# Optimization experiments

Hardware: AMD Instinct MI355X
Metric: run time of the kernel (lower is better)

Reference implementation:

```python
import jax, jax.numpy as jnp
import numpy as np

# Loihi CUBA neuron constants (from netParams['neuron']):
# threshold theta = vThMant * 2^6, decays out of 4096, weighted input scaled by 2^6.
THETA = 80.0 * 64.0
I_DECAY = 1024.0
V_DECAY = 128.0
W_SCALE = 64.0
SURR_BETA = THETA  # width of surrogate-gradient window (SLAYER-style exp pdf)

@jax.custom_jvp
def spike_fn(v):
    return (v >= THETA).astype(v.dtype)

@spike_fn.defjvp
def spike_fn_jvp(primals, tangents):
    (v,), (dv,) = primals, tangents
    s = (v >= THETA).astype(v.dtype)
    grad = jnp.exp(-jnp.abs(v - THETA) / SURR_BETA) / SURR_BETA
    return s, grad * dv

def loihi_neuron(wx):
    """Leaky integrate-and-fire (Loihi CUBA) dynamics over time.
    wx: (B, C, T) weighted input; returns (B, C, T) spikes."""
    a_i = (4096.0 - I_DECAY) / 4096.0
    a_v = (4096.0 - V_DECAY) / 4096.0
    xT = jnp.moveaxis(wx, -1, 0)  # (T, B, C)
    def step(carry, x_t):
        cur, vol = carry
        cur = a_i * cur + W_SCALE * x_t
        vol = a_v * vol + cur
        s = spike_fn(vol)
        vol = vol * (1.0 - s)  # reset on spike (refDelay = 1)
        return (cur, vol), s
    z = jnp.zeros(xT.shape[1:], wx.dtype)
    _, sT = jax.lax.scan(step, (z, z), xT)
    return jnp.moveaxis(sT, 0, -1)

def delay_shift(s, d=1):
    # shift spikes by d time steps (axonal delay), zero-padded at t=0
    zeros = jnp.zeros(s.shape[:-1] + (d,), s.dtype)
    return jnp.concatenate([zeros, s[..., :-d]], axis=-1)

def setup_inputs() -> dict:
    key = jax.random.key(0)
    k1, k2, k3 = jax.random.split(key, 3)
    B, Nin, Nhid, Nout, T = 64, 512, 1024, 512, 1024
    x = (jax.random.uniform(k1, (B, Nin, T)) < 0.1).astype(jnp.float32)
    w1 = jax.random.normal(k2, (Nhid, Nin), jnp.float32) * 0.3
    w2 = jax.random.normal(k3, (Nout, Nhid), jnp.float32) * 0.3
    return {"x": x, "w1": w1, "w2": w2}

def reference(x, w1, w2):
    h = jnp.einsum('bit,hi->bht', x, w1)           # fc1 per time step
    s1 = delay_shift(loihi_neuron(h), 1)            # spikeLoihi + delayShift(1)
    o = jnp.einsum('bht,oh->bot', s1, w2)           # fc2 per time step
    return delay_shift(loihi_neuron(o), 1)
```

## Files before the change

kernel.cpp:

```cpp
#include <hip/hip_runtime.h>
#include <stdint.h>

#define NB   64
#define NIN  512
#define NHID 1024
#define NOUT 512
#define NT   1024

#define LSTRIDE 128

#define A_I   0.75f
#define A_V   0.96875f
#define WSC   64.0f
#define THETA 5120.0f

typedef uint32_t u32x4 __attribute__((ext_vector_type(4)));
typedef uint32_t u32x2 __attribute__((ext_vector_type(2)));

#define GL4(DST, PTR, OFF) \
  asm volatile("global_load_dwordx4 %0, %1, off offset:" OFF : "=v"(DST) : "v"(PTR))
#define GL2(DST, PTR) \
  asm volatile("global_load_dwordx2 %0, %1, off" : "=v"(DST) : "v"(PTR))
#define GL1(DST, PTR) \
  asm volatile("global_load_dword %0, %1, off" : "=v"(DST) : "v"(PTR))

#define LDS_FENCE() asm volatile("s_waitcnt lgkmcnt(0)" ::: "memory")

__global__ void __launch_bounds__(256) k_bits1(const float* __restrict__ x,
                                               uint32_t* __restrict__ bits1) {
  int blk = blockIdx.x;
  int b  = blk >> 6;
  int iw = (blk >> 2) & 15;
  int tc = blk & 3;
  int t  = tc * 256 + threadIdx.x;
  const float* xp = x + ((size_t)(b * NIN + iw * 32)) * NT + t;
  uint32_t w = 0;
#pragma unroll
  for (int j = 0; j < 32; ++j) {
    float v = xp[(size_t)j * NT];
    if (v > 0.5f) w |= (1u << j);
  }
  bits1[((size_t)b * NT + t) * 16 + iw] = w;
}

__global__ void __launch_bounds__(256) k_extract(const uint64_t* __restrict__ bits,
                                                 uint32_t* __restrict__ cnt,
                                                 uint16_t* __restrict__ list,
                                                 int words, int sentinel_scaled,
                                                 int shift) {
  int gid = blockIdx.x * 256 + threadIdx.x;
  const uint64_t* wp = bits + (size_t)gid * words;
  uint16_t* lp = list + (size_t)gid * LSTRIDE;
  int c = 0;
  for (int w = 0; w < words; ++w) {
    uint64_t v = wp[w];
    while (v) {
      int j = __builtin_ctzll(v);
      v &= v - 1;
      if (c < LSTRIDE) lp[c] = (uint16_t)(((w << 6) + j) << shift);
      ++c;
    }
  }
  if (c > LSTRIDE) c = LSTRIDE;
  cnt[gid] = (uint32_t)((c + 15) >> 4);
  int cp = c;
  if (cp & 1) { lp[cp] = (uint16_t)sentinel_scaled; ++cp; }
  uint32_t s2 = (uint32_t)sentinel_scaled * 0x10001u;
  uint32_t* lp32 = (uint32_t*)lp;
  for (int k = cp >> 1; k < LSTRIDE / 2; ++k) lp32[k] = s2;
}

#define SUM16(ACC, B) do { _Pragma("unroll") \
  for (int q_ = 0; q_ < 16; ++q_) (ACC) += (B)[q_]; } while (0)
#define SUM8(ACC, B) do { _Pragma("unroll") \
  for (int q_ = 0; q_ < 8; ++q_) (ACC) += (B)[q_]; } while (0)

__global__ void __launch_bounds__(1024, 4) k_fc1(const float* __restrict__ w1,
                                                 const uint32_t* __restrict__ cnt1,
                                                 const uint16_t* __restrict__ list1,
                                                 uint64_t* __restrict__ bits2) {
  extern __shared__ float lds[];
  int xcd = blockIdx.x & 7, slot = blockIdx.x >> 3;
  int bq = (xcd << 1) | (slot & 1);
  int hq = slot >> 1;
  int h0 = hq * 64;
  for (int idx = threadIdx.x; idx < NIN * 64; idx += 1024) {
    int hl = idx >> 9;
    int i  = idx & (NIN - 1);
    lds[i * 64 + hl] = w1[(size_t)(h0 + hl) * NIN + i];
  }
  if (threadIdx.x < 64) lds[NIN * 64 + threadIdx.x] = 0.0f;
  float* stbase = lds + 32832;
  int*   flbase = (int*)(lds + 32832 + 2048);
  stbase[threadIdx.x]        = 0.0f;
  stbase[1024 + threadIdx.x] = 0.0f;
  if (threadIdx.x < 16)
    flbase[threadIdx.x] = (int)(threadIdx.x >> 2) - 4;
  __syncthreads();

  int wid = threadIdx.x >> 6, lane = threadIdx.x & 63;
  int c   = wid & 3;
  int par = wid >> 2;
  int b = bq * 4 + c;
  size_t bt = (size_t)b * NT;
  float2* stMine = (float2*)(stbase + (par * 4 + c) * 128);
  float2* stPart = (float2*)(stbase + (((par + 3) & 3) * 4 + c) * 128);
  volatile int* flMine = flbase + par * 4 + c;
  volatile int* flPart = flbase + ((par + 3) & 3) * 4 + c;

  float P[16], Q[16], R[16];
  u32x4 ct[8], rt[8];
  int cntC;
  {
    const u32x4* Lp = (const u32x4*)(list1 + (bt + par) * LSTRIDE);
#pragma unroll
    for (int k = 0; k < 8; ++k) ct[k] = Lp[k];
    cntC = (int)cnt1[bt + par];
  }

#define FC1_LOADG(BUF, CA_, CB_) do {                                           \
    u32x4 ca_ = (CA_), cb_ = (CB_);                                             \
    BUF[0]  = lds[(ca_[0] & 0xffffu) + lane];                                   \
    BUF[1]  = lds[(ca_[0] >> 16)     + lane];                                   \
    BUF[2]  = lds[(ca_[1] & 0xffffu) + lane];                                   \
    BUF[3]  = lds[(ca_[1] >> 16)     + lane];                                   \
    BUF[4]  = lds[(ca_[2] & 0xffffu) + lane];                                   \
    BUF[5]  = lds[(ca_[2] >> 16)     + lane];                                   \
    BUF[6]  = lds[(ca_[3] & 0xffffu) + lane];                                   \
    BUF[7]  = lds[(ca_[3] >> 16)     + lane];                                   \
    BUF[8]  = lds[(cb_[0] & 0xffffu) + lane];                                   \
    BUF[9]  = lds[(cb_[0] >> 16)     + lane];                                   \
    BUF[10] = lds[(cb_[1] & 0xffffu) + lane];                                   \
    BUF[11] = lds[(cb_[1] >> 16)     + lane];                                   \
    BUF[12] = lds[(cb_[2] & 0xffffu) + lane];                                   \
    BUF[13] = lds[(cb_[2] >> 16)     + lane];                                   \
    BUF[14] = lds[(cb_[3] & 0xffffu) + lane];                                   \
    BUF[15] = lds[(cb_[3] >> 16)     + lane];                                   \
  } while (0)

#define FC1_JOIN(RT, CW)                                                        \
    asm volatile("s_waitcnt vmcnt(0)"                                           \
      : "+v"(RT[0]), "+v"(RT[1]), "+v"(RT[2]), "+v"(RT[3]),                     \
        "+v"(RT[4]), "+v"(RT[5]), "+v"(RT[6]), "+v"(RT[7]), "+v"(CW)            \
      :: "memory")

#define FC1_BODY(T, CT, RT) do {                                                \
    const int t_ = (T);                                                         \
    int tp_ = t_ + 4;  if (tp_ > NT - 1) tp_ = NT - 1;                          \
    const uint16_t* lp_ = list1 + (bt + tp_) * LSTRIDE;                         \
    const uint32_t* cp_ = cnt1 + (bt + tp_);                                    \
    uint32_t cw_;                                                               \
    GL1(cw_, cp_);                                                              \
    GL4(RT[0], lp_, "0");   GL4(RT[1], lp_, "16");                              \
    GL4(RT[2], lp_, "32");  GL4(RT[3], lp_, "48");                              \
    GL4(RT[4], lp_, "64");  GL4(RT[5], lp_, "80");                              \
    GL4(RT[6], lp_, "96");  GL4(RT[7], lp_, "112");                             \
    int ng_ = __builtin_amdgcn_readfirstlane(cntC);                             \
    float acc = 0.f;                                                            \
        \
    FC1_LOADG(P, CT[0], CT[1]);                                                 \
    FC1_LOADG(Q, CT[2], CT[3]);                                                 \
    SUM16(acc, P);                                                              \
    FC1_LOADG(R, CT[4], CT[5]);                                                 \
    SUM16(acc, Q);                                                              \
    FC1_LOADG(P, CT[6], CT[7]);                                                 \
    SUM16(acc, R);                                                              \
    SUM16(acc, P);                                                              \
    if (__builtin_expect(ng_ > 4, 0)) {                 \
      const u32x4* Lc_ = (const u32x4*)(list1 + (bt + t_) * LSTRIDE);           \
      for (int g = 4; g < ng_; ++g) {                                           \
        u32x4 x0 = Lc_[2 * g], x1 = Lc_[2 * g + 1];                             \
        FC1_LOADG(R, x0, x1);                                                   \
        SUM16(acc, R);                                                          \
      }                                                                         \
    }                                                                           \
    FC1_JOIN(RT, cw_);                                                          \
       \
    {                                                                           \
      int want_ = t_ - 1;                                                       \
      for (;;) {                                                                \
        int fl_ = *flPart;                                                      \
        if (fl_ >= want_) break;                                                \
        __builtin_amdgcn_s_sleep(1);                                            \
      }                                                                         \
      LDS_FENCE();                                                              \
      float2 sv_ = stPart[lane];                                                \
      float cur_ = A_I * sv_.x + WSC * acc;                                     \
      float vol_ = A_V * sv_.y + cur_;                                          \
      bool s_ = vol_ >= THETA;                                                  \
      vol_ = s_ ? 0.f : vol_;                                                   \
      stMine[lane] = make_float2(cur_, vol_);                                   \
      LDS_FENCE();                                                              \
      if (lane == 0) *flMine = t_;                                              \
      unsigned long long m_ = __ballot(s_);                                     \
      if (lane == 0) bits2[(bt + t_) * 16 + hq] = m_;                           \
    }                                                                           \
    cntC = (int)cw_;                                                            \
  } while (0)

  for (int k = 0; k < 128; ++k) {
    FC1_BODY(par + 8 * k,     ct, rt);
    FC1_BODY(par + 8 * k + 4, rt, ct);
  }
#undef FC1_BODY
#undef FC1_LOADG
#undef FC1_JOIN
}

__global__ void __launch_bounds__(256, 1) k_fc2(const float* __restrict__ w2,
                                                const uint32_t* __restrict__ cnt2,
                                                const uint16_t* __restrict__ list2,
                                                float* __restrict__ out) {
  extern __shared__ float lds[];
  int xcd = blockIdx.x & 7, slot = blockIdx.x >> 3;
  int bq = (xcd << 1) | (slot & 1);
  int oq = slot >> 1;
  int o0 = oq * 32;
  for (int idx = threadIdx.x; idx < NHID * 32; idx += 256) {
    int om = idx >> 10;
    int i  = idx & (NHID - 1);
    lds[i * 32 + om] = w2[(size_t)(o0 + om) * NHID + i];
  }
  if (threadIdx.x < 32) lds[NHID * 32 + threadIdx.x] = 0.0f;
  __syncthreads();

  int wid = threadIdx.x >> 6, lane = threadIdx.x & 63;
  int col = lane & 31;
  int sh  = (lane >> 5) << 4;
  int b = bq * 4 + wid;
  size_t bt = (size_t)b * NT;
  float* op = out + ((size_t)b * NOUT + o0 + col) * NT;

  float cur = 0.f, vol = 0.f;
  uint32_t sm = 0;
  float P[8], Q[8], R[8];
  u32x4 cA[4], cB[4], rA[4], rB[4];
  u32x2 cN, rN;

#define FC2_LOADG(BUF, CA_, CB_) do {                                           \
    u32x4 ca_ = (CA_), cb_ = (CB_);                                             \
    BUF[0] = lds[((ca_[0] >> sh) & 0xffffu) + col];                             \
    BUF[1] = lds[((ca_[1] >> sh) & 0xffffu) + col];                             \
    BUF[2] = lds[((ca_[2] >> sh) & 0xffffu) + col];                             \
    BUF[3] = lds[((ca_[3] >> sh) & 0xffffu) + col];                             \
    BUF[4] = lds[((cb_[0] >> sh) & 0xffffu) + col];                             \
    BUF[5] = lds[((cb_[1] >> sh) & 0xffffu) + col];                             \
    BUF[6] = lds[((cb_[2] >> sh) & 0xffffu) + col];                             \
    BUF[7] = lds[((cb_[3] >> sh) & 0xffffu) + col];                             \
  } while (0)

#define FC2_JOIN(RA, RB, RN)                                                    \
    asm volatile("s_waitcnt vmcnt(0)"                                           \
      : "+v"(RA[0]), "+v"(RA[1]), "+v"(RA[2]), "+v"(RA[3]),                     \
        "+v"(RB[0]), "+v"(RB[1]), "+v"(RB[2]), "+v"(RB[3]), "+v"(RN)            \
      :: "memory")

#define FC2_FLUSH(PV) do {                                                      \
    if (lane < 32) {                                                            \
      float vb[16];                                                             \
      _Pragma("unroll")                                                         \
      for (int q = 0; q < 16; ++q) vb[q] = ((sm >> q) & 1u) ? 1.0f : 0.0f;      \
      float4* dst = (float4*)(op + ((PV) - 15));                                \
      dst[0] = make_float4(vb[0],  vb[1],  vb[2],  vb[3]);                      \
      dst[1] = make_float4(vb[4],  vb[5],  vb[6],  vb[7]);                      \
      dst[2] = make_float4(vb[8],  vb[9],  vb[10], vb[11]);                     \
      dst[3] = make_float4(vb[12], vb[13], vb[14], vb[15]);                     \
    }                                                                           \
  } while (0)

#pragma unroll
  for (int k = 0; k < 4; ++k)
    cA[k] = (u32x4){0x80008000u, 0x80008000u, 0x80008000u, 0x80008000u};
  {
    const u32x4* Lz = (const u32x4*)(list2 + bt * LSTRIDE);
#pragma unroll
    for (int k = 0; k < 4; ++k) cB[k] = Lz[k];
    cN[0] = 0; cN[1] = cnt2[bt];
  }
  FC2_LOADG(P, cA[0], cA[1]);
  FC2_LOADG(Q, cB[0], cB[1]);

#define FC2_BODY(TAU, CA, CB, CN, RA, RB, RN) do {                              \
    const int tau_ = (TAU);                                                     \
    const uint16_t* lp_ = list2 + (bt + tau_ + 1) * LSTRIDE;                    \
    const uint32_t* cp_ = cnt2 + (bt + tau_ + 1);                               \
    GL4(RA[0], lp_, "0");   GL4(RA[1], lp_, "16");                              \
    GL4(RA[2], lp_, "32");  GL4(RA[3], lp_, "48");                              \
    GL4(RB[0], lp_, "256"); GL4(RB[1], lp_, "272");                             \
    GL4(RB[2], lp_, "288"); GL4(RB[3], lp_, "304");                             \
    GL2(RN, cp_);                                                               \
    float accA = 0.f, accB = 0.f;                                               \
    FC2_LOADG(R, CA[2], CA[3]);  SUM8(accA, P);                                 \
    FC2_LOADG(P, CB[2], CB[3]);  SUM8(accB, Q);                                 \
    SUM8(accA, R);  SUM8(accB, P);                                              \
    int ngA_ = __builtin_amdgcn_readfirstlane((int)CN[0]);                      \
    int ngB_ = __builtin_amdgcn_readfirstlane((int)CN[1]);                      \
    int gmx_ = ngA_ > ngB_ ? ngA_ : ngB_;                                       \
    if (__builtin_expect(gmx_ > 2, 0)) {          \
      const u32x4* LsA_ = (const u32x4*)(list2 + (bt + tau_) * LSTRIDE) - 16;   \
      const u32x4* LsB_ = LsA_ + 16;                                            \
      for (int g = 2; g < gmx_; ++g) {                                          \
        if (g < ngA_) { u32x4 x0 = LsA_[2*g], x1 = LsA_[2*g+1];                 \
                        FC2_LOADG(R, x0, x1); SUM8(accA, R); }                  \
        if (g < ngB_) { u32x4 x0 = LsB_[2*g], x1 = LsB_[2*g+1];                 \
                        FC2_LOADG(R, x0, x1); SUM8(accB, R); }                  \
      }                                                                         \
    }                                                                           \
    FC2_JOIN(RA, RB, RN);                                                       \
    FC2_LOADG(P, RA[0], RA[1]);                                                 \
    FC2_LOADG(Q, RB[0], RB[1]);                                                 \
    accA += __shfl_xor(accA, 32, 64);         \
    cur = A_I * cur + WSC * accA;                                               \
    vol = A_V * vol + cur;                                                      \
    bool sA_ = vol >= THETA;  vol = sA_ ? 0.f : vol;                            \
    int pA_ = tau_ + 1;                                                         \
    if (sA_) sm |= 1u << (pA_ & 15);                                            \
    if ((pA_ & 15) == 15) { FC2_FLUSH(pA_); sm = 0; }                           \
    accB += __shfl_xor(accB, 32, 64);                                           \
    cur = A_I * cur + WSC * accB;                                               \
    vol = A_V * vol + cur;                                                      \
    bool sB_ = vol >= THETA;  vol = sB_ ? 0.f : vol;                            \
    int pB_ = tau_ + 2;                                                         \
    if (sB_) sm |= 1u << (pB_ & 15);                                            \
               \
  } while (0)

  for (int tau = 0; tau < 1020; tau += 4) {
    FC2_BODY(tau,     cA, cB, cN, rA, rB, rN);
    FC2_BODY(tau + 2, rA, rB, rN, cA, cB, cN);
  }
  FC2_BODY(1020, cA, cB, cN, rA, rB, rN);
  {
    int ng_ = __builtin_amdgcn_readfirstlane((int)rN[0]);
    float accA = 0.f;
    FC2_LOADG(R, rA[2], rA[3]);
    SUM8(accA, P);
    SUM8(accA, R);
    if (__builtin_expect(ng_ > 2, 0)) {
      const u32x4* Ls_ = (const u32x4*)(list2 + (bt + 1021) * LSTRIDE);
      for (int g = 2; g < ng_; ++g) {
        u32x4 x0 = Ls_[2 * g], x1 = Ls_[2 * g + 1];
        FC2_LOADG(R, x0, x1); SUM8(accA, R);
      }
    }
    accA += __shfl_xor(accA, 32, 64);
    cur = A_I * cur + WSC * accA;
    vol = A_V * vol + cur;
    bool s_ = vol >= THETA;
    if (s_) sm |= 1u << 15;
    FC2_FLUSH(1023);
  }
#undef FC2_BODY
#undef FC2_LOADG
#undef FC2_JOIN
#undef FC2_FLUSH
}

extern "C" void kernel_launch(void* const* d_in, const int* in_sizes, int n_in,
                              void* d_out, int out_size, void* d_ws, size_t ws_size,
                              hipStream_t stream) {
  const float* x  = (const float*)d_in[0];
  const float* w1 = (const float*)d_in[1];
  const float* w2 = (const float*)d_in[2];
  float* out = (float*)d_out;

  char* ws = (char*)d_ws;
  uint32_t* bits1 = (uint32_t*)(ws);
  uint32_t* cnt1  = (uint32_t*)(ws + 4194304);
  uint16_t* list1 = (uint16_t*)(ws + 4456448);
  uint64_t* bits2 = (uint64_t*)(ws + 21233664);
  uint32_t* cnt2  = (uint32_t*)(ws + 29622272);
  uint16_t* list2 = (uint16_t*)(ws + 29884416);

  const int LDS1 = (513 * 64 + 2048 + 16) * 4;
  const int LDS2 = (NHID + 1) * 32 * 4;
  (void)hipFuncSetAttribute((const void*)k_fc1,
      hipFuncAttributeMaxDynamicSharedMemorySize, LDS1);
  (void)hipFuncSetAttribute((const void*)k_fc2,
      hipFuncAttributeMaxDynamicSharedMemorySize, LDS2);

  k_bits1 <<<NB * 16 * 4, 256, 0, stream>>>(x, bits1);
  k_extract<<<(NB * NT) / 256, 256, 0, stream>>>((const uint64_t*)bits1, cnt1,
                                                 list1, 8, NIN << 6, 6);
  k_fc1   <<<16 * 16, 1024, LDS1, stream>>>(w1, cnt1, list1, bits2);
  k_extract<<<(NB * NT) / 256, 256, 0, stream>>>((const uint64_t*)bits2, cnt2,
                                                 list2, 16, NHID << 5, 5);
  k_fc2   <<<16 * 16, 256, LDS2, stream>>>(w2, cnt2, list2, out);
}
```

Before: 841.2 us.

## Split fc2 timesteps across four wave phases with LDS state handoff

k_fc2 now launches 1024 threads per block instead of 256. The 16 waves form 4 phase groups per batch row, and each group handles every fourth timestep. The sparse weighted sums are gathered in parallel across phases, while the serial LIF recurrence is handed off through LDS state and polled flags, mirroring the fc1 design. Spike bits from the four phases are merged in LDS before the float output is written. This adds spin-wait synchronisation and a larger LDS footprint, in exchange for hiding gather latency behind more waves in flight.

```diff
diff --git a/kernel.cpp b/kernel.cpp
--- a/kernel.cpp
+++ b/kernel.cpp
@@ -19,8 +19,6 @@
 
 #define GL4(DST, PTR, OFF) \
   asm volatile("global_load_dwordx4 %0, %1, off offset:" OFF : "=v"(DST) : "v"(PTR))
-#define GL2(DST, PTR) \
-  asm volatile("global_load_dwordx2 %0, %1, off" : "=v"(DST) : "v"(PTR))
 #define GL1(DST, PTR) \
   asm volatile("global_load_dword %0, %1, off" : "=v"(DST) : "v"(PTR))
 
@@ -207,35 +205,65 @@
 #undef FC1_JOIN
 }
 
-__global__ void __launch_bounds__(256, 1) k_fc2(const float* __restrict__ w2,
-                                                const uint32_t* __restrict__ cnt2,
-                                                const uint16_t* __restrict__ list2,
-                                                float* __restrict__ out) {
+__global__ void __launch_bounds__(1024, 4) k_fc2(const float* __restrict__ w2,
+                                                 const uint32_t* __restrict__ cnt2,
+                                                 const uint16_t* __restrict__ list2,
+                                                 float* __restrict__ out) {
   extern __shared__ float lds[];
   int xcd = blockIdx.x & 7, slot = blockIdx.x >> 3;
   int bq = (xcd << 1) | (slot & 1);
   int oq = slot >> 1;
   int o0 = oq * 32;
-  for (int idx = threadIdx.x; idx < NHID * 32; idx += 256) {
+  for (int idx = threadIdx.x; idx < NHID * 32; idx += 1024) {
     int om = idx >> 10;
     int i  = idx & (NHID - 1);
     lds[i * 32 + om] = w2[(size_t)(o0 + om) * NHID + i];
   }
   if (threadIdx.x < 32) lds[NHID * 32 + threadIdx.x] = 0.0f;
+  float*    stbase = lds + 32800;
+  int*      flbase = (int*)(lds + 32800 + 2048);
+  uint32_t* smwbase = (uint32_t*)(lds + 32800 + 2048 + 16);
+  stbase[threadIdx.x]        = 0.0f;
+  stbase[1024 + threadIdx.x] = 0.0f;
+  if (threadIdx.x < 16)
+    flbase[threadIdx.x] = (int)(threadIdx.x >> 2) - 4;
+  if (threadIdx.x < 512) smwbase[threadIdx.x] = 0u;
   __syncthreads();
 
   int wid = threadIdx.x >> 6, lane = threadIdx.x & 63;
+  int c   = wid & 3;
+  int par = wid >> 2;
   int col = lane & 31;
   int sh  = (lane >> 5) << 4;
-  int b = bq * 4 + wid;
+  int b = bq * 4 + c;
   size_t bt = (size_t)b * NT;
   float* op = out + ((size_t)b * NOUT + o0 + col) * NT;
-
-  float cur = 0.f, vol = 0.f;
+  int lastpos = (par == 3) ? 12 : par + 13;
+
+  float2* stMine = (float2*)(stbase + (par * 4 + c) * 128);
+  float2* stPart = (float2*)(stbase + (((par + 3) & 3) * 4 + c) * 128);
+  volatile int* flMine = flbase + par * 4 + c;
+  volatile int* flPart = flbase + ((par + 3) & 3) * 4 + c;
+  uint32_t* smwMine = smwbase + (par * 4 + c) * 32;
+  const uint32_t* smw0 = smwbase + (0 * 4 + c) * 32;
+  const uint32_t* smw1 = smwbase + (1 * 4 + c) * 32;
+  const uint32_t* smw3 = smwbase + (3 * 4 + c) * 32;
+
   uint32_t sm = 0;
-  float P[8], Q[8], R[8];
-  u32x4 cA[4], cB[4], rA[4], rB[4];
-  u32x2 cN, rN;
+  float P[8], R[8];
+  u32x4 ct[4], rt[4];
+  int cntC;
+  if (par == 0) {
+#pragma unroll
+    for (int k = 0; k < 4; ++k)
+      ct[k] = (u32x4){0x80008000u, 0x80008000u, 0x80008000u, 0x80008000u};
+    cntC = 0;
+  } else {
+    const u32x4* Lz = (const u32x4*)(list2 + (bt + par - 1) * LSTRIDE);
+#pragma unroll
+    for (int k = 0; k < 4; ++k) ct[k] = Lz[k];
+    cntC = (int)cnt2[bt + par - 1];
+  }
 
 #define FC2_LOADG(BUF, CA_, CB_) do {                                           \
     u32x4 ca_ = (CA_), cb_ = (CB_);                                             \
@@ -249,111 +277,87 @@
     BUF[7] = lds[((cb_[3] >> sh) & 0xffffu) + col];                             \
   } while (0)
 
-#define FC2_JOIN(RA, RB, RN)                                                    \
+#define FC2_JOIN(RT, CW)                                                        \
     asm volatile("s_waitcnt vmcnt(0)"                                           \
-      : "+v"(RA[0]), "+v"(RA[1]), "+v"(RA[2]), "+v"(RA[3]),                     \
-        "+v"(RB[0]), "+v"(RB[1]), "+v"(RB[2]), "+v"(RB[3]), "+v"(RN)            \
+      : "+v"(RT[0]), "+v"(RT[1]), "+v"(RT[2]), "+v"(RT[3]), "+v"(CW)            \
       :: "memory")
 
-#define FC2_FLUSH(PV) do {                                                      \
-    if (lane < 32) {                                                            \
-      float vb[16];                                                             \
-      _Pragma("unroll")                                                         \
-      for (int q = 0; q < 16; ++q) vb[q] = ((sm >> q) & 1u) ? 1.0f : 0.0f;      \
-      float4* dst = (float4*)(op + ((PV) - 15));                                \
-      dst[0] = make_float4(vb[0],  vb[1],  vb[2],  vb[3]);                      \
-      dst[1] = make_float4(vb[4],  vb[5],  vb[6],  vb[7]);                      \
-      dst[2] = make_float4(vb[8],  vb[9],  vb[10], vb[11]);                     \
-      dst[3] = make_float4(vb[12], vb[13], vb[14], vb[15]);                     \
+  FC2_LOADG(P, ct[0], ct[1]);
+
+#define FC2_BODY(T, CT, RT) do {                                                \
+    const int t_ = (T);                                                         \
+    int tp_ = t_ + 3;  if (tp_ > NT - 1) tp_ = NT - 1;                          \
+    const uint16_t* lp_ = list2 + (bt + tp_) * LSTRIDE;                         \
+    const uint32_t* cp_ = cnt2 + (bt + tp_);                                    \
+    uint32_t cw_;                                                               \
+    GL1(cw_, cp_);                                                              \
+    GL4(RT[0], lp_, "0");  GL4(RT[1], lp_, "16");                               \
+    GL4(RT[2], lp_, "32"); GL4(RT[3], lp_, "48");                               \
+    int ng_ = __builtin_amdgcn_readfirstlane(cntC);                             \
+    float acc = 0.f;                                                            \
+    FC2_LOADG(R, CT[2], CT[3]);                                                 \
+    SUM8(acc, P);                                                               \
+    SUM8(acc, R);                                                               \
+    if (__builtin_expect(ng_ > 2, 0)) {           \
+      const u32x4* Ls_ = (const u32x4*)(list2 + (bt + t_ - 1) * LSTRIDE);       \
+      for (int g = 2; g < ng_; ++g) {                                           \
+        u32x4 x0 = Ls_[2 * g], x1 = Ls_[2 * g + 1];                             \
+        FC2_LOADG(R, x0, x1);                                                   \
+        SUM8(acc, R);                                                           \
+      }                                                                         \
     }                                                                           \
+    FC2_JOIN(RT, cw_);                                                          \
+    FC2_LOADG(P, RT[0], RT[1]);          \
+    acc += __shfl_xor(acc, 32, 64);           \
+    {                                                                           \
+      int want_ = t_ - 1;                                                       \
+      for (;;) {                                                                \
+        int fl_ = *flPart;                                                      \
+        if (fl_ >= want_) break;                                                \
+        __builtin_amdgcn_s_sleep(1);                                            \
+      }                                                                         \
+      LDS_FENCE();                                                              \
+      float2 sv_ = stPart[lane];                                                \
+      float cur_ = A_I * sv_.x + WSC * acc;                                     \
+      float vol_ = A_V * sv_.y + cur_;                                          \
+      bool s_ = vol_ >= THETA;                                                  \
+      vol_ = s_ ? 0.f : vol_;                                                   \
+      stMine[lane] = make_float2(cur_, vol_);                                   \
+      int p_ = t_ + 1;                                                          \
+      int pos_ = p_ & 15;                                                       \
+      if (s_) sm |= 1u << pos_;                                                 \
+      uint32_t myw_ = sm;                                                       \
+      bool isLast_ = (pos_ == lastpos);                                         \
+      if (isLast_) {                                                            \
+        if (lane < 32) smwMine[col] = myw_;                                     \
+        sm = 0;                                                                 \
+      }                                                                         \
+      LDS_FENCE();                                                              \
+      if (lane == 0) *flMine = t_;                                              \
+      if (par == 2 && isLast_) {             \
+        uint32_t w_ = myw_ | smw0[col] | smw1[col] | smw3[col];                 \
+        if (lane < 32) {                                                        \
+          float vb[16];                                                         \
+          _Pragma("unroll")                                                     \
+          for (int q = 0; q < 16; ++q) vb[q] = ((w_ >> q) & 1u) ? 1.0f : 0.0f;  \
+          float4* dst = (float4*)(op + (p_ - 15));                              \
+          dst[0] = make_float4(vb[0],  vb[1],  vb[2],  vb[3]);                  \
+          dst[1] = make_float4(vb[4],  vb[5],  vb[6],  vb[7]);                  \
+          dst[2] = make_float4(vb[8],  vb[9],  vb[10], vb[11]);                 \
+          dst[3] = make_float4(vb[12], vb[13], vb[14], vb[15]);                 \
+        }                                                                       \
+      }                                                                         \
+    }                                                                           \
+    cntC = (int)cw_;                                                            \
   } while (0)
 
-#pragma unroll
-  for (int k = 0; k < 4; ++k)
-    cA[k] = (u32x4){0x80008000u, 0x80008000u, 0x80008000u, 0x80008000u};
-  {
-    const u32x4* Lz = (const u32x4*)(list2 + bt * LSTRIDE);
-#pragma unroll
-    for (int k = 0; k < 4; ++k) cB[k] = Lz[k];
-    cN[0] = 0; cN[1] = cnt2[bt];
-  }
-  FC2_LOADG(P, cA[0], cA[1]);
-  FC2_LOADG(Q, cB[0], cB[1]);
-
-#define FC2_BODY(TAU, CA, CB, CN, RA, RB, RN) do {                              \
-    const int tau_ = (TAU);                                                     \
-    const uint16_t* lp_ = list2 + (bt + tau_ + 1) * LSTRIDE;                    \
-    const uint32_t* cp_ = cnt2 + (bt + tau_ + 1);                               \
-    GL4(RA[0], lp_, "0");   GL4(RA[1], lp_, "16");                              \
-    GL4(RA[2], lp_, "32");  GL4(RA[3], lp_, "48");                              \
-    GL4(RB[0], lp_, "256"); GL4(RB[1], lp_, "272");                             \
-    GL4(RB[2], lp_, "288"); GL4(RB[3], lp_, "304");                             \
-    GL2(RN, cp_);                                                               \
-    float accA = 0.f, accB = 0.f;                                               \
-    FC2_LOADG(R, CA[2], CA[3]);  SUM8(accA, P);                                 \
-    FC2_LOADG(P, CB[2], CB[3]);  SUM8(accB, Q);                                 \
-    SUM8(accA, R);  SUM8(accB, P);                                              \
-    int ngA_ = __builtin_amdgcn_readfirstlane((int)CN[0]);                      \
-    int ngB_ = __builtin_amdgcn_readfirstlane((int)CN[1]);                      \
-    int gmx_ = ngA_ > ngB_ ? ngA_ : ngB_;                                       \
-    if (__builtin_expect(gmx_ > 2, 0)) {          \
-      const u32x4* LsA_ = (const u32x4*)(list2 + (bt + tau_) * LSTRIDE) - 16;   \
-      const u32x4* LsB_ = LsA_ + 16;                                            \
-      for (int g = 2; g < gmx_; ++g) {                                          \
-        if (g < ngA_) { u32x4 x0 = LsA_[2*g], x1 = LsA_[2*g+1];                 \
-                        FC2_LOADG(R, x0, x1); SUM8(accA, R); }                  \
-        if (g < ngB_) { u32x4 x0 = LsB_[2*g], x1 = LsB_[2*g+1];                 \
-                        FC2_LOADG(R, x0, x1); SUM8(accB, R); }                  \
-      }                                                                         \
-    }                                                                           \
-    FC2_JOIN(RA, RB, RN);                                                       \
-    FC2_LOADG(P, RA[0], RA[1]);                                                 \
-    FC2_LOADG(Q, RB[0], RB[1]);                                                 \
-    accA += __shfl_xor(accA, 32, 64);         \
-    cur = A_I * cur + WSC * accA;                                               \
-    vol = A_V * vol + cur;                                                      \
-    bool sA_ = vol >= THETA;  vol = sA_ ? 0.f : vol;                            \
-    int pA_ = tau_ + 1;                                                         \
-    if (sA_) sm |= 1u << (pA_ & 15);                                            \
-    if ((pA_ & 15) == 15) { FC2_FLUSH(pA_); sm = 0; }                           \
-    accB += __shfl_xor(accB, 32, 64);                                           \
-    cur = A_I * cur + WSC * accB;                                               \
-    vol = A_V * vol + cur;                                                      \
-    bool sB_ = vol >= THETA;  vol = sB_ ? 0.f : vol;                            \
-    int pB_ = tau_ + 2;                                                         \
-    if (sB_) sm |= 1u << (pB_ & 15);                                            \
-               \
-  } while (0)
-
-  for (int tau = 0; tau < 1020; tau += 4) {
-    FC2_BODY(tau,     cA, cB, cN, rA, rB, rN);
-    FC2_BODY(tau + 2, rA, rB, rN, cA, cB, cN);
-  }
-  FC2_BODY(1020, cA, cB, cN, rA, rB, rN);
-  {
-    int ng_ = __builtin_amdgcn_readfirstlane((int)rN[0]);
-    float accA = 0.f;
-    FC2_LOADG(R, rA[2], rA[3]);
-    SUM8(accA, P);
-    SUM8(accA, R);
-    if (__builtin_expect(ng_ > 2, 0)) {
-      const u32x4* Ls_ = (const u32x4*)(list2 + (bt + 1021) * LSTRIDE);
-      for (int g = 2; g < ng_; ++g) {
-        u32x4 x0 = Ls_[2 * g], x1 = Ls_[2 * g + 1];
-        FC2_LOADG(R, x0, x1); SUM8(accA, R);
-      }
-    }
-    accA += __shfl_xor(accA, 32, 64);
-    cur = A_I * cur + WSC * accA;
-    vol = A_V * vol + cur;
-    bool s_ = vol >= THETA;
-    if (s_) sm |= 1u << 15;
-    FC2_FLUSH(1023);
+  for (int k = 0; k < 128; ++k) {
+    FC2_BODY(par + 8 * k,     ct, rt);
+    FC2_BODY(par + 8 * k + 4, rt, ct);
   }
 #undef FC2_BODY
 #undef FC2_LOADG
 #undef FC2_JOIN
-#undef FC2_FLUSH
 }
 
 extern "C" void kernel_launch(void* const* d_in, const int* in_sizes, int n_in,
@@ -373,7 +377,7 @@
   uint16_t* list2 = (uint16_t*)(ws + 29884416);
 
   const int LDS1 = (513 * 64 + 2048 + 16) * 4;
-  const int LDS2 = (NHID + 1) * 32 * 4;
+  const int LDS2 = (32800 + 2048 + 16 + 512) * 4;
   (void)hipFuncSetAttribute((const void*)k_fc1,
       hipFuncAttributeMaxDynamicSharedMemorySize, LDS1);
   (void)hipFuncSetAttribute((const void*)k_fc2,
@@ -385,5 +389,5 @@
   k_fc1   <<<16 * 16, 1024, LDS1, stream>>>(w1, cnt1, list1, bits2);
   k_extract<<<(NB * NT) / 256, 256, 0, stream>>>((const uint64_t*)bits2, cnt2,
                                                  list2, 16, NHID << 5, 5);
-  k_fc2   <<<16 * 16, 256, LDS2, stream>>>(w2, cnt2, list2, out);
-}
+  k_fc2   <<<16 * 16, 1024, LDS2, stream>>>(w2, cnt2, list2, out);
+}
```

New measurement: 769.8 us. 8.5% less time.
